# Kernel optimization log

Hardware: AMD Instinct MI355X
Metric: run time of the kernel (lower is better)

## Reference

```python
import jax, jax.numpy as jnp
import numpy as np

B, S, D = 8, 1024, 576
H, HD = 9, 64
LAT = 144
FF = 1536
N_ROUTED, TOP_K = 7, 2
EPS = 1e-5
THETA = 10000.0


def setup_inputs() -> dict:
    key = jax.random.key(0)
    ks = jax.random.split(key, 20)
    sc = lambda fan_in: 1.0 / np.sqrt(fan_in)
    inp = {
        "x": jax.random.normal(ks[0], (B, S, D), jnp.float32),
        "ln1_w": jnp.ones((D,), jnp.float32),
        "ln2_w": jnp.ones((D,), jnp.float32),
        # attention projections, torch Linear layout (out, in)
        "Wqd": jax.random.normal(ks[1], (LAT, D), jnp.float32) * sc(D),
        "Wkvd": jax.random.normal(ks[2], (LAT, D), jnp.float32) * sc(D),
        "Wqu": jax.random.normal(ks[3], (D, LAT), jnp.float32) * sc(LAT),
        "Wku": jax.random.normal(ks[4], (D, LAT), jnp.float32) * sc(LAT),
        "Wvu": jax.random.normal(ks[5], (D, LAT), jnp.float32) * sc(LAT),
        "Wo": jax.random.normal(ks[6], (D, D), jnp.float32) * sc(D),
        # shared expert SwiGLU
        "sg": jax.random.normal(ks[7], (FF, D), jnp.float32) * sc(D),
        "su": jax.random.normal(ks[8], (FF, D), jnp.float32) * sc(D),
        "sd": jax.random.normal(ks[9], (D, FF), jnp.float32) * sc(FF),
        # routed experts, stacked [E, out, in]
        "rg": jax.random.normal(ks[10], (N_ROUTED, FF, D), jnp.float32) * sc(D),
        "ru": jax.random.normal(ks[11], (N_ROUTED, FF, D), jnp.float32) * sc(D),
        "rd": jax.random.normal(ks[12], (N_ROUTED, D, FF), jnp.float32) * sc(FF),
        "Wr": jax.random.normal(ks[13], (N_ROUTED, D), jnp.float32) * sc(D),
        "rb": jnp.zeros((N_ROUTED,), jnp.float32),
    }
    return inp


def _rmsnorm(x, w, eps=EPS):
    xf = x.astype(jnp.float32)
    y = xf * jax.lax.rsqrt(jnp.mean(xf * xf, axis=-1, keepdims=True) + eps)
    return y.astype(x.dtype) * w


def _rotate_half(x):
    x1, x2 = x[..., : x.shape[-1] // 2], x[..., x.shape[-1] // 2 :]
    return jnp.concatenate((-x2, x1), axis=-1)


def _rope(q, k, seq_len):
    inv_freq = 1.0 / THETA ** (jnp.arange(0, HD, 2, dtype=jnp.float32) / HD)
    freqs = jnp.arange(seq_len, dtype=jnp.float32)[:, None] * inv_freq  # [S, HD/2]
    emb = jnp.concatenate((freqs, freqs), axis=-1)  # [S, HD]
    cos = jnp.cos(emb)[None, None, :, :]
    sin = jnp.sin(emb)[None, None, :, :]
    return q * cos + _rotate_half(q) * sin, k * cos + _rotate_half(k) * sin


def _swiglu(h, Wg, Wu, Wd):
    return (jax.nn.silu(h @ Wg.T) * (h @ Wu.T)) @ Wd.T


def reference(x, ln1_w, ln2_w, Wqd, Wkvd, Wqu, Wku, Wvu, Wo,
              sg, su, sd, rg, ru, rd, Wr, rb):
    bsz, seq_len, _ = x.shape
    # ---- attention sublayer ----
    residual = x
    h = _rmsnorm(x, ln1_w)
    q_lat = h @ Wqd.T
    kv_lat = h @ Wkvd.T
    q = (q_lat @ Wqu.T).reshape(bsz, seq_len, H, HD).transpose(0, 2, 1, 3)
    k = (kv_lat @ Wku.T).reshape(bsz, seq_len, H, HD).transpose(0, 2, 1, 3)
    v = (kv_lat @ Wvu.T).reshape(bsz, seq_len, H, HD).transpose(0, 2, 1, 3)
    q, k = _rope(q, k, seq_len)
    scores = jnp.einsum("bhqd,bhkd->bhqk", q, k) / jnp.sqrt(jnp.float32(HD))
    causal = jnp.tril(jnp.ones((seq_len, seq_len), bool))
    scores = jnp.where(causal, scores, jnp.float32(-jnp.inf))
    attn = jax.nn.softmax(scores, axis=-1)
    o = jnp.einsum("bhqk,bhkd->bhqd", attn, v).transpose(0, 2, 1, 3).reshape(bsz, seq_len, D)
    x = residual + o @ Wo.T
    # ---- MoE sublayer ----
    residual = x
    h = _rmsnorm(x, ln2_w)
    shared = _swiglu(h, sg, su, sd)  # 1 shared expert
    logits = h @ Wr.T + rb
    probs = jax.nn.sigmoid(logits)
    scores_k, idx = jax.lax.top_k(probs, TOP_K)  # [B,S,K]
    scores_k = scores_k / jnp.sum(scores_k, axis=-1, keepdims=True)
    # per-token weight for each routed expert [B,S,E]
    w = jnp.sum(jax.nn.one_hot(idx, N_ROUTED, dtype=h.dtype) * scores_k[..., None], axis=-2)
    combined = jnp.zeros_like(h)
    for e in range(N_ROUTED):  # small fixed expert count
        combined = combined + w[..., e : e + 1] * _swiglu(h, rg[e], ru[e], rd[e])
    return residual + shared + combined
```

## Files before the change

kernel.cpp:

```cpp
#include <hip/hip_runtime.h>
#include <stdint.h>
#include <math.h>

#define B_    8
#define S_    1024
#define D_    576
#define H_    9
#define HD_   64
#define LAT_  144
#define FF_   1536
#define NE_   7
#define NT_   8192
#define NPAIR_ 16384
#define NACT_  24576
#define MAXT_ 200

typedef unsigned short u16;
typedef __attribute__((ext_vector_type(8))) short bf16x8;
typedef __attribute__((ext_vector_type(4))) float f32x4;
typedef __attribute__((ext_vector_type(4))) unsigned short us4;

__device__ __forceinline__ u16 f2b(float f){
  union{float f;uint32_t u;} v; v.f=f;
  uint32_t u=v.u;
  return (u16)((u + 0x7fffu + ((u>>16)&1u))>>16);
}
__device__ __forceinline__ float b2f(u16 h){
  union{uint32_t u;float f;} v; v.u=((uint32_t)h)<<16; return v.f;
}

#define MFMA16(a,b,c) __builtin_amdgcn_mfma_f32_16x16x32_bf16((a),(b),(c),0,0,0)

typedef __attribute__((address_space(1))) const unsigned char g_u8;
typedef __attribute__((address_space(3))) unsigned char s_u8;
__device__ __forceinline__ void gll16(const void* g, void* l){
  __builtin_amdgcn_global_load_lds((g_u8*)g, (s_u8*)l, 16, 0, 0);
}

struct CvtSegs {
  const float* src[6];
  u16* dst[6];
  int start4[7];
};
__global__ void k_cvt(CvtSegs cs){
  int tot = cs.start4[6];
  for(int i = blockIdx.x*blockDim.x + threadIdx.x; i < tot; i += gridDim.x*blockDim.x){
    int s=0;
    #pragma unroll
    for(int j=0;j<6;j++) if(i >= cs.start4[j+1]) s=j+1;
    int loc = i - cs.start4[s];
    float4 v = ((const float4*)cs.src[s])[loc];
    us4 o; o[0]=f2b(v.x); o[1]=f2b(v.y); o[2]=f2b(v.z); o[3]=f2b(v.w);
    ((us4*)cs.dst[s])[loc] = o;
  }
}

struct CvtSegs2 {
  const float* src[3];
  u16* dhi[3]; u16* dlo[3];
  int start4[4];
};
__global__ void k_cvt_split(CvtSegs2 cs){
  int tot = cs.start4[3];
  for(int i = blockIdx.x*blockDim.x + threadIdx.x; i < tot; i += gridDim.x*blockDim.x){
    int s=0;
    #pragma unroll
    for(int j=0;j<3;j++) if(i >= cs.start4[j+1]) s=j+1;
    int loc = i - cs.start4[s];
    float4 v = ((const float4*)cs.src[s])[loc];
    us4 oh, ol;
    float vv[4]={v.x,v.y,v.z,v.w};
    #pragma unroll
    for(int j=0;j<4;j++){ u16 hh=f2b(vv[j]); oh[j]=hh; ol[j]=f2b(vv[j]-b2f(hh)); }
    ((us4*)cs.dhi[s])[loc]=oh;
    ((us4*)cs.dlo[s])[loc]=ol;
  }
}

__global__ void k_cvt_pad_split(const float* __restrict__ Wqu, const float* __restrict__ Wku,
                                const float* __restrict__ Wvu,
                                u16* __restrict__ dhi, u16* __restrict__ dlo){
  int i = blockIdx.x*256 + threadIdx.x;
  if(i >= 3*D_*160) return;
  int z = i/(D_*160); int rem = i - z*D_*160;
  int row = rem/160, col = rem - row*160;
  const float* s = (z==0)?Wqu:((z==1)?Wku:Wvu);
  float v = (col<LAT_)? s[row*LAT_+col] : 0.f;
  u16 hh=f2b(v);
  dhi[i]=hh; dlo[i]=f2b(v-b2f(hh));
}

__global__ void k_rope_tab(float* __restrict__ cost, float* __restrict__ sint){
  int i = blockIdx.x*256+threadIdx.x; if(i>=S_*32) return;
  int s=i>>5, d=i&31;
  float pw = (float)pow(10000.0, (double)d/32.0);
  float inv = 1.0f/pw;
  float ang = (float)s*inv;
  cost[i]=cosf(ang); sint[i]=sinf(ang);
}

__global__ __launch_bounds__(64) void k_rms(const float* __restrict__ x, const float* __restrict__ w,
                      u16* __restrict__ hhi, u16* __restrict__ hlo){
  int t = blockIdx.x; int lane = threadIdx.x;
  const float* xr = x + (size_t)t*D_;
  float v[9]; float ss=0.f;
  #pragma unroll
  for(int j=0;j<9;j++){ v[j]=xr[lane+64*j]; ss += v[j]*v[j]; }
  #pragma unroll
  for(int m=1;m<64;m<<=1) ss += __shfl_xor(ss,m,64);
  float sc = 1.0f/sqrtf(ss/(float)D_ + 1e-5f);
  #pragma unroll
  for(int j=0;j<9;j++){
    float y = v[j]*sc*w[lane+64*j];
    size_t o=(size_t)t*D_+lane+64*j;
    u16 hh=f2b(y); hhi[o]=hh; hlo[o]=f2b(y-b2f(hh));
  }
}

__global__ __launch_bounds__(256) void k_rms_router(const float* __restrict__ x2, const float* __restrict__ w,
                        const float* __restrict__ Wr, const float* __restrict__ rb,
                        u16* __restrict__ hb, int* __restrict__ idx2, float* __restrict__ w2){
  int wid=threadIdx.x>>6, lane=threadIdx.x&63;
  int t = blockIdx.x*4 + wid;
  const float* xr = x2 + (size_t)t*D_;
  float v[9]; float ss=0.f;
  #pragma unroll
  for(int j=0;j<9;j++){ v[j]=xr[lane+64*j]; ss += v[j]*v[j]; }
  #pragma unroll
  for(int m=1;m<64;m<<=1) ss += __shfl_xor(ss,m,64);
  float sc = 1.0f/sqrtf(ss/(float)D_ + 1e-5f);
  float hv[9];
  #pragma unroll
  for(int j=0;j<9;j++){
    float y = v[j]*sc*w[lane+64*j];
    hv[j]=y;
    hb[(size_t)t*D_+lane+64*j]=f2b(y);
  }
  float pr[7];
  #pragma unroll
  for(int e=0;e<7;e++){
    float s=0.f;
    #pragma unroll
    for(int j=0;j<9;j++) s += hv[j]*Wr[e*D_+lane+64*j];
    #pragma unroll
    for(int mm=1;mm<64;mm<<=1) s+=__shfl_xor(s,mm,64);
    pr[e] = 1.f/(1.f+expf(-(s+rb[e])));
  }
  int e0=0; float b0=pr[0];
  #pragma unroll
  for(int e=1;e<7;e++) if(pr[e]>b0){b0=pr[e];e0=e;}
  int e1=-1; float b1=-1e30f;
  #pragma unroll
  for(int e=0;e<7;e++) if(e!=e0 && pr[e]>b1){b1=pr[e];e1=e;}
  if(lane==0){
    float s=b0+b1;
    idx2[2*t]=e0; idx2[2*t+1]=e1;
    w2[2*t]=b0/s; w2[2*t+1]=b1/s;
  }
}

template<int EPI>
__global__ __launch_bounds__(256) void k_gemm2(
    const u16* __restrict__ Ahi, const u16* __restrict__ Alo, int lda, int aofs_z,
    const u16* __restrict__ Bhi, const u16* __restrict__ Blo, int ldb, long bStrideZ,
    int N, int ksteps,
    u16* __restrict__ Chi, u16* __restrict__ Clo, int ldc,
    float* __restrict__ C32, long cStrideZ, const float* __restrict__ resid)
{
  __shared__ u16 Ahs[128*32], Als[128*32], Bhs[128*32], Bls[128*32];
  int tid=threadIdx.x, wid=tid>>6, lane=tid&63;
  int m0=blockIdx.x*128, n0=blockIdx.y*128, z=blockIdx.z;
  const u16* Abh = Ahi + ((z>0)?aofs_z:0);
  const u16* Abl = Alo + ((z>0)?aofs_z:0);
  const u16* Bbh = Bhi + (long)z*bStrideZ;
  const u16* Bbl = Blo + (long)z*bStrideZ;
  int lq=lane&15, lg=lane>>4;
  int wr=wid>>1, wc=wid&1;
  f32x4 acc[4][4]={};
  for(int kt=0;kt<ksteps;kt++){
    #pragma unroll
    for(int is=0;is<2;is++){
      int ub = is*4096 + wid*1024;
      int o = ub + lane*16;
      int row = o>>6, p=(o>>4)&3;
      int sc8 = ((p ^ ((row>>1)&3)))*8;
      long aoff = (long)(m0+row)*lda + kt*32 + sc8;
      gll16(Abh+aoff, (char*)Ahs+ub);
      gll16(Abl+aoff, (char*)Als+ub);
      int rowb = n0+row; rowb = rowb<N?rowb:(N-1);
      long boff = (long)rowb*ldb + kt*32 + sc8;
      gll16(Bbh+boff, (char*)Bhs+ub);
      gll16(Bbl+boff, (char*)Bls+ub);
    }
    __syncthreads();
    bf16x8 ah[4], al[4], bh[4], bl[4];
    #pragma unroll
    for(int m=0;m<4;m++){
      int arow=wr*64+m*16+lq;
      int co = arow*32 + ((lg ^ ((arow>>1)&3)))*8;
      ah[m]=*(const bf16x8*)&Ahs[co];
      al[m]=*(const bf16x8*)&Als[co];
    }
    #pragma unroll
    for(int n=0;n<4;n++){
      int brow=wc*64+n*16+lq;
      int co = brow*32 + ((lg ^ ((brow>>1)&3)))*8;
      bh[n]=*(const bf16x8*)&Bhs[co];
      bl[n]=*(const bf16x8*)&Bls[co];
    }
    #pragma unroll
    for(int m=0;m<4;m++)
      #pragma unroll
      for(int n=0;n<4;n++){
        acc[m][n]=MFMA16(ah[m],bh[n],acc[m][n]);
        acc[m][n]=MFMA16(ah[m],bl[n],acc[m][n]);
        acc[m][n]=MFMA16(al[m],bh[n],acc[m][n]);
      }
    __syncthreads();
  }
  #pragma unroll
  for(int m=0;m<4;m++){
    #pragma unroll
    for(int n=0;n<4;n++){
      int col = n0 + wc*64 + n*16 + lq;
      if(col<N){
        #pragma unroll
        for(int r=0;r<4;r++){
          int row = m0 + wr*64 + m*16 + lg*4 + r;
          float val = acc[m][n][r];
          if(EPI==0){
            int dc = (col<144)? col : col+16;
            u16 hh=f2b(val);
            Chi[(long)row*ldc + dc] = hh;
            Clo[(long)row*ldc + dc] = f2b(val-b2f(hh));
          } else if(EPI==1){
            (C32 + (long)z*cStrideZ)[(long)row*ldc + col] = val;
          } else {
            C32[(long)row*ldc+col] = resid[(long)row*ldc+col] + val;
          }
        }
      }
    }
  }
}

__global__ void k_ropesplit(const float* __restrict__ QR, const float* __restrict__ KR,
                            const float* __restrict__ cost, const float* __restrict__ sint,
                            u16* __restrict__ QHI, u16* __restrict__ QLO,
                            u16* __restrict__ KHI, u16* __restrict__ KLO){
  int i = blockIdx.x*256+threadIdx.x;
  if(i >= NT_*H_*32) return;
  int d = i&31; int h=(i>>5)%H_; int t = i/(H_*32);
  int s = t & (S_-1); int b = t >> 10;
  float c = cost[s*32+d], sn = sint[s*32+d];
  long qi = (long)t*D_ + h*HD_ + d;
  float q1=QR[qi], q2=QR[qi+32];
  float k1=KR[qi], k2=KR[qi+32];
  long ob = ((long)(b*H_+h)*S_ + s)*HD_ + d;
  float qa=(q1*c - q2*sn)*0.125f, qb2=(q2*c + q1*sn)*0.125f;
  float ka=k1*c - k2*sn,          kb2=k2*c + k1*sn;
  u16 hh;
  hh=f2b(qa);  QHI[ob]=hh;    QLO[ob]   =f2b(qa -b2f(hh));
  hh=f2b(qb2); QHI[ob+32]=hh; QLO[ob+32]=f2b(qb2-b2f(hh));
  hh=f2b(ka);  KHI[ob]=hh;    KLO[ob]   =f2b(ka -b2f(hh));
  hh=f2b(kb2); KHI[ob+32]=hh; KLO[ob+32]=f2b(kb2-b2f(hh));
}

__global__ __launch_bounds__(256) void k_vsplit(const float* __restrict__ VR,
                       u16* __restrict__ VHI, u16* __restrict__ VLO){
  __shared__ float ls[64][65];
  int s0 = blockIdx.x*64; int bh = blockIdx.y;
  int b = bh/H_, h = bh - b*H_;
  int tid=threadIdx.x;
  #pragma unroll
  for(int i=0;i<16;i++){
    int idx = tid + i*256;
    int si = idx>>6, dj = idx&63;
    ls[si][dj] = VR[((long)(b*S_+s0+si))*D_ + h*HD_ + dj];
  }
  __syncthreads();
  #pragma unroll
  for(int i=0;i<16;i++){
    int idx = tid + i*256;
    int di = idx>>6, sj = idx&63;
    float v = ls[sj][di];
    u16 hh = f2b(v);
    long o = ((long)bh*HD_+di)*S_ + s0+sj;
    VHI[o]=hh; VLO[o]=f2b(v-b2f(hh));
  }
}

__global__ __launch_bounds__(256) void k_attn_split(
    const u16* __restrict__ QHI, const u16* __restrict__ QLO,
    const u16* __restrict__ KHI, const u16* __restrict__ KLO,
    const u16* __restrict__ VHI, const u16* __restrict__ VLO,
    u16* __restrict__ OHI, u16* __restrict__ OLO){
  __shared__ u16 lds[2][4][64*64];
  int tid=threadIdx.x, wid=tid>>6, lane=tid&63;
  int bh=blockIdx.x; int b=bh/H_, h=bh-b*H_;
  int jb=blockIdx.y;
  int lq=lane&15, lg=lane>>4;
  int jslot=lane&7, rloc=lane>>3;

  for(int pass=0;pass<2;pass++){
    int tile = pass? (15-jb) : jb;
    int ntile = tile+1;
    int q0 = tile*64 + wid*16;
    long qoff = ((long)bh*S_ + q0+lq)*HD_;
    bf16x8 qh0 = *(const bf16x8*)(QHI+qoff+lg*8);
    bf16x8 qh1 = *(const bf16x8*)(QHI+qoff+32+lg*8);
    bf16x8 ql0 = *(const bf16x8*)(QLO+qoff+lg*8);
    bf16x8 ql1 = *(const bf16x8*)(QLO+qoff+32+lg*8);
    float m=-1e30f, l=0.f;
    f32x4 ot[4]={};
    int q_lane = q0 + lq;

    #define STAGE(bufi, kv0_) do{                                          \
      int _kv0=(kv0_);                                                     \
      _Pragma("unroll")                                                    \
      for(int c=0;c<2;c++){                                                \
        int r = wid*16 + c*8 + rloc;                                       \
        int col = 8*(jslot ^ (r&7));                                       \
        long kg = ((long)bh*S_ + _kv0 + r)*64 + col;                       \
        long vg = ((long)bh*64 + r)*S_ + _kv0 + col;                       \
        int lb = (wid*16 + c*8)*64;                                        \
        gll16(KHI+kg, &lds[bufi][0][lb]);                                  \
        gll16(KLO+kg, &lds[bufi][1][lb]);                                  \
        gll16(VHI+vg, &lds[bufi][2][lb]);                                  \
        gll16(VLO+vg, &lds[bufi][3][lb]);                                  \
      } }while(0)

    STAGE(0, 0);
    __syncthreads();
    for(int t=0;t<ntile;t++){
      if(t+1<ntile) STAGE((t+1)&1, (t+1)*64);
      int bufc = t&1;
      int kv0 = t*64;
      bool last = (t==ntile-1);
      const char* Khs=(const char*)lds[bufc][0];
      const char* Kls=(const char*)lds[bufc][1];
      const char* Vhs=(const char*)lds[bufc][2];
      const char* Vls=(const char*)lds[bufc][3];
      #pragma unroll
      for(int kvh=0;kvh<64;kvh+=32){
        float p[8];
        float tmax=-1e30f;
        #pragma unroll
        for(int sub=0;sub<2;sub++){
          int r = kvh + sub*16 + lq;
          int sw = (r&7)<<4;
          bf16x8 kh0=*(const bf16x8*)(Khs + r*128 + ((lg*16) ^ sw));
          bf16x8 kh1=*(const bf16x8*)(Khs + r*128 + ((64+lg*16) ^ sw));
          bf16x8 kl0=*(const bf16x8*)(Kls + r*128 + ((lg*16) ^ sw));
          bf16x8 kl1=*(const bf16x8*)(Kls + r*128 + ((64+lg*16) ^ sw));
          f32x4 st={0.f,0.f,0.f,0.f};
          st=MFMA16(kh0,qh0,st); st=MFMA16(kh1,qh1,st);
          st=MFMA16(kl0,qh0,st); st=MFMA16(kl1,qh1,st);
          st=MFMA16(kh0,ql0,st); st=MFMA16(kh1,ql1,st);
          #pragma unroll
          for(int r2=0;r2<4;r2++){
            int key = kv0 + kvh + sub*16 + lg*4 + r2;
            float sv = (!last || key <= q_lane)? st[r2] : -1e30f;
            p[sub*4+r2]=sv;
            tmax = fmaxf(tmax, sv);
          }
        }
        tmax = fmaxf(tmax, __shfl_xor(tmax,16,64));
        tmax = fmaxf(tmax, __shfl_xor(tmax,32,64));
        float mn = fmaxf(m, tmax);
        float sc = __expf(m - mn);
        l *= sc;
        #pragma unroll
        for(int t2=0;t2<4;t2++)
          #pragma unroll
          for(int r2=0;r2<4;r2++) ot[t2][r2]*=sc;
        float ps=0.f;
        #pragma unroll
        for(int j=0;j<8;j++){ p[j]=__expf(p[j]-mn); ps+=p[j]; }
        l+=ps; m=mn;
        bf16x8 ph, pl;
        #pragma unroll
        for(int j=0;j<8;j++){
          u16 hb2=f2b(p[j]);
          ph[j]=(short)hb2;
          pl[j]=(short)f2b(p[j]-b2f(hb2));
        }
        #pragma unroll
        for(int t2=0;t2<4;t2++){
          int d = t2*16+lq;
          int swd = (d&7)<<4;
          int b1 = (2*(kvh+4*lg)) ^ swd;
          int b2v = (2*(kvh+16+4*lg)) ^ swd;
          us4 vh0=*(const us4*)(Vhs + d*128 + b1);
          us4 vh1=*(const us4*)(Vhs + d*128 + b2v);
          us4 vl0=*(const us4*)(Vls + d*128 + b1);
          us4 vl1=*(const us4*)(Vls + d*128 + b2v);
          bf16x8 vh, vl;
          #pragma unroll
          for(int j=0;j<4;j++){
            vh[j]=(short)vh0[j]; vh[4+j]=(short)vh1[j];
            vl[j]=(short)vl0[j]; vl[4+j]=(short)vl1[j];
          }
          ot[t2]=MFMA16(vh,ph,ot[t2]);
          ot[t2]=MFMA16(vl,ph,ot[t2]);
          ot[t2]=MFMA16(vh,pl,ot[t2]);
        }
      }
      __syncthreads();
    }
    #undef STAGE
    float l1 = l + __shfl_xor(l,16,64);
    float lt = l1 + __shfl_xor(l1,32,64);
    float inv = 1.f/lt;
    long orow = ((long)b*S_ + q_lane)*D_ + h*HD_;
    #pragma unroll
    for(int t2=0;t2<4;t2++){
      us4 oh4, ol4;
      #pragma unroll
      for(int r2=0;r2<4;r2++){
        float v=ot[t2][r2]*inv;
        u16 hh=f2b(v);
        oh4[r2]=hh; ol4[r2]=f2b(v-b2f(hh));
      }
      *(us4*)(OHI + orow + t2*16 + 4*lg) = oh4;
      *(us4*)(OLO + orow + t2*16 + 4*lg) = ol4;
    }
  }
}

__global__ __launch_bounds__(256) void k_count(const int* __restrict__ idx2, int* __restrict__ counts){
  __shared__ int hist[NE_];
  int tid=threadIdx.x;
  if(tid<NE_) hist[tid]=0;
  __syncthreads();
  int i = blockIdx.x*256+tid;
  atomicAdd(&hist[idx2[i]],1);
  __syncthreads();
  if(tid<NE_) atomicAdd(&counts[tid], hist[tid]);
}

__global__ void k_offsets(const int* __restrict__ counts, int* __restrict__ ofs,
                          int* __restrict__ fill, int* __restrict__ ts){
  if(threadIdx.x==0 && blockIdx.x==0){
    int a=0;
    for(int e=0;e<NE_;e++){ ofs[e]=a; fill[e]=a; a+=counts[e]; }
    ofs[NE_]=a;
    int t=0;
    for(int e=0;e<NE_;e++){ ts[e]=t; t += (counts[e]+127)>>7; }
    ts[NE_]=t; t+=64;
    ts[NE_+1]=t;
  }
}

__global__ __launch_bounds__(256) void k_scatter2(const int* __restrict__ idx2, const float* __restrict__ w2,
                          int* __restrict__ fill, int* __restrict__ ltok,
                          float* __restrict__ lw, int* __restrict__ ppos){
  __shared__ int wcnt[4][8];
  __shared__ int wpre[4][8];
  __shared__ int base[8];
  int tid=threadIdx.x, wid=tid>>6, lane=tid&63;
  int slot = blockIdx.x*256 + wid*64 + lane;
  int id = idx2[slot];
  unsigned long long ltm = (1ull<<lane)-1ull;
  int myrank=0;
  #pragma unroll
  for(int e=0;e<7;e++){
    unsigned long long mask = __ballot(id==e);
    if(id==e) myrank = __popcll(mask & ltm);
    if(lane==0) wcnt[wid][e] = __popcll(mask);
  }
  __syncthreads();
  if(wid==0 && lane<7){
    int e=lane;
    int s0=wcnt[0][e], s1=wcnt[1][e], s2=wcnt[2][e], s3=wcnt[3][e];
    wpre[0][e]=0; wpre[1][e]=s0; wpre[2][e]=s0+s1; wpre[3][e]=s0+s1+s2;
    base[e] = atomicAdd(&fill[e], s0+s1+s2+s3);
  }
  __syncthreads();
  int pos = base[id] + wpre[wid][id] + myrank;
  ltok[pos] = slot>>1;
  lw[pos] = w2[slot];
  ppos[slot] = pos;
}

__global__ __launch_bounds__(256) void k_moe_gu(const u16* __restrict__ h2b, const u16* __restrict__ Gb,
                        const u16* __restrict__ Ub, const int* __restrict__ cnt,
                        const int* __restrict__ ofs, const int* __restrict__ ts,
                        const int* __restrict__ ltok, u16* __restrict__ act){
  int tsv[9];
  #pragma unroll
  for(int i=0;i<9;i++) tsv[i]=ts[i];
  int xt = blockIdx.y;
  if(xt >= tsv[8]) return;
  int e=0;
  #pragma unroll
  for(int i=1;i<8;i++) if(xt >= tsv[i]) e=i;
  int mt = xt - tsv[e];
  int nrows = (e<NE_)? cnt[e] : NT_;
  int base  = (e<NE_)? ofs[e] : 0;
  long arow0 = (e<NE_)? (long)base : (long)NPAIR_;
  int f0 = blockIdx.x*128;
  __shared__ u16 As[2][128*32], Gs[2][128*32], Us[2][128*32];
  int tid=threadIdx.x, wid=tid>>6, lane=tid&63;
  int lq=lane&15, lg=lane>>4;
  int wr=wid>>1, wc=wid&1;
  int r0 = wid*16 + (lane>>2);
  int r1 = 64 + r0;
  int so = wid*1024 + lane*16;
  int sc8 = ((lane&3) ^ ((r0>>1)&3))*8;
  int ri0 = mt*128+r0; if(ri0>nrows-1) ri0=nrows-1;
  int ri1 = mt*128+r1; if(ri1>nrows-1) ri1=nrows-1;
  long tok0 = (e<NE_)? (long)ltok[base+ri0] : (long)ri0;
  long tok1 = (e<NE_)? (long)ltok[base+ri1] : (long)ri1;
  const u16* a0 = h2b + tok0*D_ + sc8;
  const u16* a1 = h2b + tok1*D_ + sc8;
  const u16* g0 = Gb + ((long)e*FF_ + f0 + r0)*D_ + sc8;
  const u16* g1 = Gb + ((long)e*FF_ + f0 + r1)*D_ + sc8;
  const u16* u0 = Ub + ((long)e*FF_ + f0 + r0)*D_ + sc8;
  const u16* u1 = Ub + ((long)e*FF_ + f0 + r1)*D_ + sc8;
  #define STG(bi, kt_) do{ int ko=(kt_)*32;                       \
    gll16(a0+ko, (char*)As[bi]+so);                               \
    gll16(a1+ko, (char*)As[bi]+4096+so);                          \
    gll16(g0+ko, (char*)Gs[bi]+so);                               \
    gll16(g1+ko, (char*)Gs[bi]+4096+so);                          \
    gll16(u0+ko, (char*)Us[bi]+so);                               \
    gll16(u1+ko, (char*)Us[bi]+4096+so); }while(0)
  f32x4 ag_[4][4]={}, au_[4][4]={};
  STG(0,0);
  __syncthreads();
  for(int kt=0;kt<18;kt++){
    int cur = kt&1;
    if(kt<17) STG(cur^1, kt+1);
    bf16x8 af[4], gf[4], uf[4];
    #pragma unroll
    for(int m=0;m<4;m++){
      int arow=wr*64+m*16+lq;
      af[m]=*(const bf16x8*)&As[cur][arow*32 + ((lg ^ ((arow>>1)&3)))*8];
    }
    #pragma unroll
    for(int n=0;n<4;n++){
      int grow=wc*64+n*16+lq;
      int co = grow*32 + ((lg ^ ((grow>>1)&3)))*8;
      gf[n]=*(const bf16x8*)&Gs[cur][co];
      uf[n]=*(const bf16x8*)&Us[cur][co];
    }
    #pragma unroll
    for(int m=0;m<4;m++)
      #pragma unroll
      for(int n=0;n<4;n++){
        ag_[m][n]=MFMA16(af[m],gf[n],ag_[m][n]);
        au_[m][n]=MFMA16(af[m],uf[n],au_[m][n]);
      }
    __syncthreads();
  }
  #undef STG
  #pragma unroll
  for(int m=0;m<4;m++){
    #pragma unroll
    for(int n=0;n<4;n++){
      int f = f0 + wc*64+n*16+lq;
      #pragma unroll
      for(int r=0;r<4;r++){
        int rl = wr*64+m*16+lg*4+r;
        int ridx = mt*128+rl;
        if(ridx<nrows){
          float g=ag_[m][n][r], u=au_[m][n][r];
          float sw = g/(1.f+__expf(-g))*u;
          act[(arow0+ridx)*FF_ + f] = f2b(sw);
        }
      }
    }
  }
}

__global__ __launch_bounds__(256) void k_moe_down(const u16* __restrict__ act, const u16* __restrict__ Db,
                          const int* __restrict__ cnt, const int* __restrict__ ofs,
                          const int* __restrict__ ts, const float* __restrict__ lw,
                          u16* __restrict__ pd){
  int tsv[9];
  #pragma unroll
  for(int i=0;i<9;i++) tsv[i]=ts[i];
  int xt = blockIdx.y;
  if(xt >= tsv[8]) return;
  int e=0;
  #pragma unroll
  for(int i=1;i<8;i++) if(xt >= tsv[i]) e=i;
  int mt = xt - tsv[e];
  int nrows=(e<NE_)?cnt[e]:NT_;
  long arow0=(e<NE_)?(long)ofs[e]:(long)NPAIR_;
  int n0=blockIdx.x*128;
  __shared__ u16 As[2][128*32], Bs[2][128*32];
  int tid=threadIdx.x,wid=tid>>6,lane=tid&63;
  int lq=lane&15,lg=lane>>4;
  int wr=wid>>1,wc=wid&1;
  int r0 = wid*16 + (lane>>2);
  int r1 = 64 + r0;
  int so = wid*1024 + lane*16;
  int sc8 = ((lane&3) ^ ((r0>>1)&3))*8;
  int ri0 = mt*128+r0; if(ri0>nrows-1) ri0=nrows-1;
  int ri1 = mt*128+r1; if(ri1>nrows-1) ri1=nrows-1;
  const u16* a0 = act + (arow0+ri0)*FF_ + sc8;
  const u16* a1 = act + (arow0+ri1)*FF_ + sc8;
  int rb0 = n0+r0; if(rb0>D_-1) rb0=D_-1;
  int rb1 = n0+r1; if(rb1>D_-1) rb1=D_-1;
  const u16* b0p = Db + ((long)e*D_ + rb0)*FF_ + sc8;
  const u16* b1p = Db + ((long)e*D_ + rb1)*FF_ + sc8;
  #define STG(bi, kt_) do{ int ko=(kt_)*32;                       \
    gll16(a0+ko, (char*)As[bi]+so);                               \
    gll16(a1+ko, (char*)As[bi]+4096+so);                          \
    gll16(b0p+ko, (char*)Bs[bi]+so);                              \
    gll16(b1p+ko, (char*)Bs[bi]+4096+so); }while(0)
  f32x4 acc[4][4]={};
  STG(0,0);
  __syncthreads();
  for(int kt=0;kt<48;kt++){
    int cur = kt&1;
    if(kt<47) STG(cur^1, kt+1);
    bf16x8 af[4],bf2[4];
    #pragma unroll
    for(int m=0;m<4;m++){
      int arow=wr*64+m*16+lq;
      af[m]=*(const bf16x8*)&As[cur][arow*32 + ((lg ^ ((arow>>1)&3)))*8];
    }
    #pragma unroll
    for(int n=0;n<4;n++){
      int brow=wc*64+n*16+lq;
      bf2[n]=*(const bf16x8*)&Bs[cur][brow*32 + ((lg ^ ((brow>>1)&3)))*8];
    }
    #pragma unroll
    for(int m=0;m<4;m++)
      #pragma unroll
      for(int n=0;n<4;n++)
        acc[m][n]=MFMA16(af[m],bf2[n],acc[m][n]);
    __syncthreads();
  }
  #undef STG
  #pragma unroll
  for(int m=0;m<4;m++){
    #pragma unroll
    for(int n=0;n<4;n++){
      int col=n0+wc*64+n*16+lq;
      if(col<D_){
        #pragma unroll
        for(int r=0;r<4;r++){
          int rl=wr*64+m*16+lg*4+r;
          int ridx=mt*128+rl;
          if(ridx<nrows){
            float w=1.f;
            if(e<NE_) w=lw[arow0+ridx];
            pd[(arow0+ridx)*D_ + col]=f2b(w*acc[m][n][r]);
          }
        }
      }
    }
  }
}

__global__ void k_final(const float* __restrict__ x2, const u16* __restrict__ pd,
                        const int* __restrict__ ppos, float* __restrict__ out){
  int i=blockIdx.x*256+threadIdx.x;
  int tot = NT_*(D_/4);
  if(i>=tot) return;
  int t = i/(D_/4); int c = (i - t*(D_/4))*4;
  int p0=ppos[2*t], p1=ppos[2*t+1];
  const u16* a=pd+((long)NPAIR_+t)*D_+c;
  const u16* b=pd+(long)p0*D_+c;
  const u16* d=pd+(long)p1*D_+c;
  const float* xr = x2+(long)t*D_+c;
  float* o = out+(long)t*D_+c;
  #pragma unroll
  for(int j=0;j<4;j++) o[j]=xr[j]+b2f(a[j])+b2f(b[j])+b2f(d[j]);
}

extern "C" void kernel_launch(void* const* d_in, const int* in_sizes, int n_in,
                              void* d_out, int out_size, void* d_ws, size_t ws_size,
                              hipStream_t stream){
  const float* x    =(const float*)d_in[0];
  const float* ln1  =(const float*)d_in[1];
  const float* ln2  =(const float*)d_in[2];
  const float* Wqd  =(const float*)d_in[3];
  const float* Wkvd =(const float*)d_in[4];
  const float* Wqu  =(const float*)d_in[5];
  const float* Wku  =(const float*)d_in[6];
  const float* Wvu  =(const float*)d_in[7];
  const float* Wo   =(const float*)d_in[8];
  const float* sg   =(const float*)d_in[9];
  const float* su   =(const float*)d_in[10];
  const float* sd   =(const float*)d_in[11];
  const float* rg   =(const float*)d_in[12];
  const float* ru   =(const float*)d_in[13];
  const float* rd   =(const float*)d_in[14];
  const float* Wr   =(const float*)d_in[15];
  const float* rb   =(const float*)d_in[16];
  float* out=(float*)d_out;

  char* ws=(char*)d_ws;
  size_t off=0;
  auto alloc=[&](size_t bsz){ size_t r=off; off=(off+bsz+255)&~(size_t)255; return r; };
  u16* GB   =(u16*)(ws+alloc(8L*FF_*D_*2));
  u16* UB   =(u16*)(ws+alloc(8L*FF_*D_*2));
  u16* DB   =(u16*)(ws+alloc(8L*D_*FF_*2));
  float* COS=(float*)(ws+alloc(S_*32*4));
  float* SIN=(float*)(ws+alloc(S_*32*4));
  float* X2 =(float*)(ws+alloc((long)NT_*D_*4));
  u16* H2B  =(u16*)(ws+alloc((long)NT_*D_*2));
  int* IDX2 =(int*)(ws+alloc(NT_*2*4));
  float* W2 =(float*)(ws+alloc(NT_*2*4));
  int* PPOS =(int*)(ws+alloc(NT_*2*4));
  int* CNT  =(int*)(ws+alloc(64));
  int* OFS  =(int*)(ws+alloc(64));
  int* FILL =(int*)(ws+alloc(64));
  int* TS   =(int*)(ws+alloc(64));
  int* LTOK =(int*)(ws+alloc(NPAIR_*4));
  float* LW =(float*)(ws+alloc(NPAIR_*4));
  size_t scr0 = off;
  const long NQ = (long)B_*H_*S_*HD_;
  u16* H1HI=(u16*)(ws+alloc((long)NT_*D_*2));
  u16* H1LO=(u16*)(ws+alloc((long)NT_*D_*2));
  u16* LATHI=(u16*)(ws+alloc((long)NT_*320*2));
  u16* LATLO=(u16*)(ws+alloc((long)NT_*320*2));
  float* QR =(float*)(ws+alloc((long)NT_*D_*4));
  float* KR =(float*)(ws+alloc((long)NT_*D_*4));
  float* VR =(float*)(ws+alloc((long)NT_*D_*4));
  u16* QHI =(u16*)(ws+alloc(NQ*2));
  u16* QLO =(u16*)(ws+alloc(NQ*2));
  u16* KHI =(u16*)(ws+alloc(NQ*2));
  u16* KLO =(u16*)(ws+alloc(NQ*2));
  u16* WDHI=(u16*)(ws+alloc(288L*D_*2));
  u16* WDLO=(u16*)(ws+alloc(288L*D_*2));
  u16* WUPHI=(u16*)(ws+alloc(3L*D_*160*2));
  u16* WUPLO=(u16*)(ws+alloc(3L*D_*160*2));
  u16* WOHI=(u16*)(ws+alloc((long)D_*D_*2));
  u16* WOLO=(u16*)(ws+alloc((long)D_*D_*2));
  u16* VHI = (u16*)QR;
  u16* VLO = (u16*)QR + NQ;
  u16* OHI = H1HI;
  u16* OLO = H1LO;
  off = scr0;
  u16* ACT =(u16*)(ws+alloc((long)NACT_*FF_*2));
  u16* PD  =(u16*)(ws+alloc((long)NACT_*D_*2));
  (void)ws_size;

  CvtSegs cs;
  {
    const float* ss[6]={rg,sg,ru,su,rd,sd};
    u16* dd[6]={GB, GB+7L*FF_*D_, UB, UB+7L*FF_*D_, DB, DB+7L*D_*FF_};
    long nn[6]={7L*FF_*D_,(long)FF_*D_,7L*FF_*D_,(long)FF_*D_,7L*D_*FF_,(long)D_*FF_};
    cs.start4[0]=0;
    for(int j=0;j<6;j++){ cs.src[j]=ss[j]; cs.dst[j]=dd[j]; cs.start4[j+1]=cs.start4[j]+(int)(nn[j]/4); }
  }
  k_cvt<<<2048,256,0,stream>>>(cs);
  CvtSegs2 c2;
  {
    const float* ss[3]={Wqd, Wkvd, Wo};
    u16* dh[3]={WDHI, WDHI+144L*D_, WOHI};
    u16* dl[3]={WDLO, WDLO+144L*D_, WOLO};
    long nn[3]={144L*D_, 144L*D_, (long)D_*D_};
    c2.start4[0]=0;
    for(int j=0;j<3;j++){ c2.src[j]=ss[j]; c2.dhi[j]=dh[j]; c2.dlo[j]=dl[j]; c2.start4[j+1]=c2.start4[j]+(int)(nn[j]/4); }
  }
  k_cvt_split<<<512,256,0,stream>>>(c2);
  k_cvt_pad_split<<<(3*D_*160+255)/256,256,0,stream>>>(Wqu,Wku,Wvu,WUPHI,WUPLO);
  k_rope_tab<<<(S_*32+255)/256,256,0,stream>>>(COS,SIN);

  k_rms<<<NT_,64,0,stream>>>(x, ln1, H1HI, H1LO);
  k_gemm2<0><<<dim3(64,3,1),256,0,stream>>>(H1HI,H1LO,D_,0, WDHI,WDLO,D_,0, 288,18, LATHI,LATLO,320, nullptr,0,nullptr);
  k_gemm2<1><<<dim3(64,5,3),256,0,stream>>>(LATHI,LATLO,320,160, WUPHI,WUPLO,160,(long)D_*160, D_,5, nullptr,nullptr,D_, QR,(long)NT_*D_, nullptr);
  k_ropesplit<<<(NT_*H_*32+255)/256,256,0,stream>>>(QR,KR,COS,SIN,QHI,QLO,KHI,KLO);
  k_vsplit<<<dim3(16,72),256,0,stream>>>(VR,VHI,VLO);
  k_attn_split<<<dim3(72,8),256,0,stream>>>(QHI,QLO,KHI,KLO,VHI,VLO,OHI,OLO);
  k_gemm2<2><<<dim3(64,5,1),256,0,stream>>>(OHI,OLO,D_,0, WOHI,WOLO,D_,0, D_,18, nullptr,nullptr,D_, X2,0, x);

  hipMemsetAsync(CNT,0,64,stream);
  k_rms_router<<<NT_/4,256,0,stream>>>(X2, ln2, Wr, rb, H2B, IDX2, W2);
  k_count<<<NPAIR_/256,256,0,stream>>>(IDX2,CNT);
  k_offsets<<<1,1,0,stream>>>(CNT,OFS,FILL,TS);
  k_scatter2<<<NPAIR_/256,256,0,stream>>>(IDX2,W2,FILL,LTOK,LW,PPOS);
  k_moe_gu<<<dim3(12,MAXT_),256,0,stream>>>(H2B,GB,UB,CNT,OFS,TS,LTOK,ACT);
  k_moe_down<<<dim3(5,MAXT_),256,0,stream>>>(ACT,DB,CNT,OFS,TS,LW,PD);
  k_final<<<(NT_*(D_/4)+255)/256,256,0,stream>>>(X2,PD,PPOS,out);
}
```

Measured before the change: 658.0 us.

## Double-buffer split-bf16 GEMM and use partial vmcnt waits in MoE GEMMs

The split-precision k_gemm2 kernel gets double-buffered shared memory, so the next K tile's global-to-LDS loads are issued before the current tile is computed. In all three GEMM loops, the full __syncthreads drain is replaced by an s_waitcnt vmcnt(N) that waits only for the current tile's loads, followed by a raw s_barrier. This lets prefetches stay in flight across the MFMA work and removes the memory stall that came with each barrier. In exchange, k_gemm2 doubles its LDS use (64KB), which may lower occupancy, and correctness now depends on the hand-counted vmcnt values matching the number of loads issued.

Result: slower. 726.1 us (+10.3%).

```diff
diff --git a/kernel.cpp b/kernel.cpp
--- a/kernel.cpp
+++ b/kernel.cpp
@@ -167,7 +167,7 @@
     u16* __restrict__ Chi, u16* __restrict__ Clo, int ldc,
     float* __restrict__ C32, long cStrideZ, const float* __restrict__ resid)
 {
-  __shared__ u16 Ahs[128*32], Als[128*32], Bhs[128*32], Bls[128*32];
+  __shared__ u16 Ahs[2][128*32], Als[2][128*32], Bhs[2][128*32], Bls[2][128*32];
   int tid=threadIdx.x, wid=tid>>6, lane=tid&63;
   int m0=blockIdx.x*128, n0=blockIdx.y*128, z=blockIdx.z;
   const u16* Abh = Ahi + ((z>0)?aofs_z:0);
@@ -176,37 +176,50 @@
   const u16* Bbl = Blo + (long)z*bStrideZ;
   int lq=lane&15, lg=lane>>4;
   int wr=wid>>1, wc=wid&1;
+  int r0 = wid*16 + (lane>>2);
+  int so = wid*1024 + lane*16;
+  int sc8 = ((lane&3) ^ ((r0>>1)&3))*8;
+  const u16* pah0 = Abh + (long)(m0+r0)*lda + sc8;
+  const u16* pah1 = Abh + (long)(m0+64+r0)*lda + sc8;
+  const u16* pal0 = Abl + (long)(m0+r0)*lda + sc8;
+  const u16* pal1 = Abl + (long)(m0+64+r0)*lda + sc8;
+  int br0 = n0+r0;    if(br0>N-1) br0=N-1;
+  int br1 = n0+64+r0; if(br1>N-1) br1=N-1;
+  const u16* pbh0 = Bbh + (long)br0*ldb + sc8;
+  const u16* pbh1 = Bbh + (long)br1*ldb + sc8;
+  const u16* pbl0 = Bbl + (long)br0*ldb + sc8;
+  const u16* pbl1 = Bbl + (long)br1*ldb + sc8;
+  #define STG(bi, kt_) do{ int ko=(kt_)*32;                \
+    gll16(pah0+ko, (char*)Ahs[bi]+so);                     \
+    gll16(pah1+ko, (char*)Ahs[bi]+4096+so);                \
+    gll16(pal0+ko, (char*)Als[bi]+so);                     \
+    gll16(pal1+ko, (char*)Als[bi]+4096+so);                \
+    gll16(pbh0+ko, (char*)Bhs[bi]+so);                     \
+    gll16(pbh1+ko, (char*)Bhs[bi]+4096+so);                \
+    gll16(pbl0+ko, (char*)Bls[bi]+so);                     \
+    gll16(pbl1+ko, (char*)Bls[bi]+4096+so); }while(0)
   f32x4 acc[4][4]={};
+  STG(0,0);
   for(int kt=0;kt<ksteps;kt++){
-    #pragma unroll
-    for(int is=0;is<2;is++){
-      int ub = is*4096 + wid*1024;
-      int o = ub + lane*16;
-      int row = o>>6, p=(o>>4)&3;
-      int sc8 = ((p ^ ((row>>1)&3)))*8;
-      long aoff = (long)(m0+row)*lda + kt*32 + sc8;
-      gll16(Abh+aoff, (char*)Ahs+ub);
-      gll16(Abl+aoff, (char*)Als+ub);
-      int rowb = n0+row; rowb = rowb<N?rowb:(N-1);
-      long boff = (long)rowb*ldb + kt*32 + sc8;
-      gll16(Bbh+boff, (char*)Bhs+ub);
-      gll16(Bbl+boff, (char*)Bls+ub);
-    }
-    __syncthreads();
+    int cur=kt&1;
+    if(kt+1<ksteps){ STG(cur^1, kt+1); asm volatile("s_waitcnt vmcnt(8)":::"memory"); }
+    else           { asm volatile("s_waitcnt vmcnt(0)":::"memory"); }
+    __builtin_amdgcn_s_barrier();
+    __builtin_amdgcn_sched_barrier(0);
     bf16x8 ah[4], al[4], bh[4], bl[4];
     #pragma unroll
     for(int m=0;m<4;m++){
       int arow=wr*64+m*16+lq;
       int co = arow*32 + ((lg ^ ((arow>>1)&3)))*8;
-      ah[m]=*(const bf16x8*)&Ahs[co];
-      al[m]=*(const bf16x8*)&Als[co];
+      ah[m]=*(const bf16x8*)&Ahs[cur][co];
+      al[m]=*(const bf16x8*)&Als[cur][co];
     }
     #pragma unroll
     for(int n=0;n<4;n++){
       int brow=wc*64+n*16+lq;
       int co = brow*32 + ((lg ^ ((brow>>1)&3)))*8;
-      bh[n]=*(const bf16x8*)&Bhs[co];
-      bl[n]=*(const bf16x8*)&Bls[co];
+      bh[n]=*(const bf16x8*)&Bhs[cur][co];
+      bl[n]=*(const bf16x8*)&Bls[cur][co];
     }
     #pragma unroll
     for(int m=0;m<4;m++)
@@ -216,8 +229,9 @@
         acc[m][n]=MFMA16(ah[m],bl[n],acc[m][n]);
         acc[m][n]=MFMA16(al[m],bh[n],acc[m][n]);
       }
-    __syncthreads();
-  }
+    __builtin_amdgcn_s_barrier();
+  }
+  #undef STG
   #pragma unroll
   for(int m=0;m<4;m++){
     #pragma unroll
@@ -527,10 +541,12 @@
     gll16(u1+ko, (char*)Us[bi]+4096+so); }while(0)
   f32x4 ag_[4][4]={}, au_[4][4]={};
   STG(0,0);
-  __syncthreads();
   for(int kt=0;kt<18;kt++){
     int cur = kt&1;
-    if(kt<17) STG(cur^1, kt+1);
+    if(kt<17){ STG(cur^1, kt+1); asm volatile("s_waitcnt vmcnt(6)":::"memory"); }
+    else     { asm volatile("s_waitcnt vmcnt(0)":::"memory"); }
+    __builtin_amdgcn_s_barrier();
+    __builtin_amdgcn_sched_barrier(0);
     bf16x8 af[4], gf[4], uf[4];
     #pragma unroll
     for(int m=0;m<4;m++){
@@ -551,7 +567,7 @@
         ag_[m][n]=MFMA16(af[m],gf[n],ag_[m][n]);
         au_[m][n]=MFMA16(af[m],uf[n],au_[m][n]);
       }
-    __syncthreads();
+    __builtin_amdgcn_s_barrier();
   }
   #undef STG
   #pragma unroll
@@ -612,10 +628,12 @@
     gll16(b1p+ko, (char*)Bs[bi]+4096+so); }while(0)
   f32x4 acc[4][4]={};
   STG(0,0);
-  __syncthreads();
   for(int kt=0;kt<48;kt++){
     int cur = kt&1;
-    if(kt<47) STG(cur^1, kt+1);
+    if(kt<47){ STG(cur^1, kt+1); asm volatile("s_waitcnt vmcnt(4)":::"memory"); }
+    else     { asm volatile("s_waitcnt vmcnt(0)":::"memory"); }
+    __builtin_amdgcn_s_barrier();
+    __builtin_amdgcn_sched_barrier(0);
     bf16x8 af[4],bf2[4];
     #pragma unroll
     for(int m=0;m<4;m++){
@@ -632,7 +650,7 @@
       #pragma unroll
       for(int n=0;n<4;n++)
         acc[m][n]=MFMA16(af[m],bf2[n],acc[m][n]);
-    __syncthreads();
+    __builtin_amdgcn_s_barrier();
   }
   #undef STG
   #pragma unroll
```
